# Kernel optimization log

Hardware: AMD Instinct MI355X
Metric: run time of the kernel (lower is better)

The kernel has to match this reference:

```python
import jax, jax.numpy as jnp
import numpy as np

N_NODES = 50000
N_EDGES = 800000
HEADS = 2
HID = 64
NEG_SLOPE = 0.2


def setup_inputs() -> dict:
    key = jax.random.key(0)
    ks = jax.random.split(key, 8)
    x = jax.random.normal(ks[0], (N_NODES, 128), dtype=jnp.float32)
    W_src = jax.random.normal(ks[1], (128, HEADS * HID), dtype=jnp.float32) * (1.0 / np.sqrt(128))
    W_dst = jax.random.normal(ks[2], (128, HEADS * HID), dtype=jnp.float32) * (1.0 / np.sqrt(128))
    att_src = jax.random.normal(ks[3], (HEADS, HID), dtype=jnp.float32) * 0.1
    att_dst = jax.random.normal(ks[4], (HEADS, HID), dtype=jnp.float32) * 0.1
    bias = jax.random.normal(ks[5], (HEADS * HID,), dtype=jnp.float32) * 0.01
    prelu_w = jnp.full((HEADS * HID,), 0.25, dtype=jnp.float32)
    edge_index = jax.random.randint(ks[6], (2, N_EDGES), 0, N_NODES, dtype=jnp.int64)
    return {"x": x, "W_src": W_src, "W_dst": W_dst, "att_src": att_src,
            "att_dst": att_dst, "bias": bias, "prelu_w": prelu_w,
            "edge_index": edge_index}


def gat_prelu(x, W_src, W_dst, att_src, att_dst, bias, prelu_w, edge_index):
    N = x.shape[0]
    src, dst = edge_index[0], edge_index[1]
    xs = (x @ W_src).reshape(N, HEADS, HID)   # [N,H,C]
    xd = (x @ W_dst).reshape(N, HEADS, HID)
    a_src = jnp.einsum('nhc,hc->nh', xs, att_src)  # [N,H]
    a_dst = jnp.einsum('nhc,hc->nh', xd, att_dst)
    e = jax.nn.leaky_relu(a_src[src] + a_dst[dst], NEG_SLOPE)  # [E,H]
    # segment softmax over incoming edges of each dst node
    m = jax.ops.segment_max(e, dst, num_segments=N)            # [N,H]
    ee = jnp.exp(e - m[dst])
    denom = jax.ops.segment_sum(ee, dst, num_segments=N)
    alpha = ee / (denom[dst] + 1e-16)                          # [E,H]
    msg = xs[src] * alpha[:, :, None]                          # [E,H,C]
    out = jax.ops.segment_sum(msg, dst, num_segments=N)        # [N,H,C]
    out = out.reshape(N, HEADS * HID) + bias
    return jnp.where(out >= 0, out, prelu_w * out)


def reference(x, W_src, W_dst, att_src, att_dst, bias, prelu_w, edge_index):
    return gat_prelu(x, W_src, W_dst, att_src, att_dst, bias, prelu_w, edge_index)
```

## Files before the change

kernel.cpp:

```cpp
#include <hip/hip_runtime.h>
#include <hip/hip_fp16.h>


#define N_NODES 50000
#define N_EDGES 800000
#define CAP     56
#define NB      49
#define CHUNK   2048
#define NBLK    391
#define CCAP    96

#define OFF_A      0
#define OFF_CNT    800000
#define OFF_XS     1000256
#define OFF_BKT    13800256
#define OFF_SWZ    36200256
#define DOUT_COARSE 0
#define DOUT_CELL   14714880

typedef _Float16 f16x8 __attribute__((ext_vector_type(8)));
typedef float    f32x4 __attribute__((ext_vector_type(4)));
typedef unsigned long long u64;

__global__ __launch_bounds__(256) void k0_prep(
    const float* __restrict__ Wsrc, const float* __restrict__ Wdst,
    const float* __restrict__ att_s, const float* __restrict__ att_d,
    __half* __restrict__ swz)
{
    __shared__ float vS[128 * 4];
    const int nt = blockIdx.x;
    const int t = threadIdx.x;
    if (nt == 8) {
        if (t < 128) {
            const float* wsp = Wsrc + t * 128;
            const float* wdp = Wdst + t * 128;
            float a0 = 0.f, a1 = 0.f, a2 = 0.f, a3 = 0.f;
#pragma unroll 8
            for (int c = 0; c < 64; ++c) {
                a0 += wsp[c]      * att_s[c];
                a1 += wsp[64 + c] * att_s[64 + c];
                a2 += wdp[c]      * att_d[c];
                a3 += wdp[64 + c] * att_d[64 + c];
            }
            *(float4*)(vS + t * 4) = make_float4(a0, a1, a2, a3);
        }
        __syncthreads();
    }
    const int kb = t >> 6, L = t & 63;
    const int col = L & 15;
    const int krow = kb * 32 + ((L >> 4) & 3) * 8;
    f16x8 v;
    if (nt < 8) {
#pragma unroll
        for (int j = 0; j < 8; ++j)
            v[j] = (_Float16)Wsrc[(size_t)(krow + j) * 128 + nt * 16 + col];
    } else {
#pragma unroll
        for (int j = 0; j < 8; ++j)
            v[j] = (col < 4) ? (_Float16)vS[(krow + j) * 4 + col] : (_Float16)0.f;
    }
    *(f16x8*)(swz + ((size_t)(kb * 9 + nt) * 64 + L) * 8) = v;
}

__global__ __launch_bounds__(256) void k1_gemm(
    const float* __restrict__ x, const __half* __restrict__ swz,
    __half* __restrict__ xs, float* __restrict__ a_all)
{
    const int t = threadIdx.x;
    const int w = t >> 6, L = t & 63;
    const int m = L & 15, q = L >> 4;
    const int n_a = blockIdx.x * 64 + w * 16 + m;
    const int rrow = (n_a < N_NODES) ? n_a : (N_NODES - 1);
    const float* xrow = x + (size_t)rrow * 128;

    f32x4 acc[9];
#pragma unroll
    for (int nt = 0; nt < 9; ++nt) acc[nt] = (f32x4){0.f, 0.f, 0.f, 0.f};

#pragma unroll
    for (int kb = 0; kb < 4; ++kb) {
        const int k0 = kb * 32 + q * 8;
        float4 xa = *(const float4*)(xrow + k0);
        float4 xb = *(const float4*)(xrow + k0 + 4);
        f16x8 a;
        a[0] = (_Float16)xa.x; a[1] = (_Float16)xa.y;
        a[2] = (_Float16)xa.z; a[3] = (_Float16)xa.w;
        a[4] = (_Float16)xb.x; a[5] = (_Float16)xb.y;
        a[6] = (_Float16)xb.z; a[7] = (_Float16)xb.w;
        const f16x8* bbase = (const f16x8*)swz + (size_t)(kb * 9) * 64 + L;
#pragma unroll
        for (int nt = 0; nt < 9; ++nt) {
            f16x8 b = bbase[(size_t)nt * 64];
            acc[nt] = __builtin_amdgcn_mfma_f32_16x16x32_f16(a, b, acc[nt], 0, 0, 0);
        }
    }

    const int rbase = blockIdx.x * 64 + w * 16 + q * 4;
#pragma unroll
    for (int nt = 0; nt < 8; ++nt) {
#pragma unroll
        for (int r = 0; r < 4; ++r) {
            int n = rbase + r;
            if (n < N_NODES)
                xs[(size_t)n * 128 + nt * 16 + m] = (__half)acc[nt][r];
        }
    }
    if (m < 4) {
#pragma unroll
        for (int r = 0; r < 4; ++r) {
            int n = rbase + r;
            if (n < N_NODES) a_all[(size_t)n * 4 + m] = acc[8][r];
        }
    }
}

__global__ __launch_bounds__(256) void kB_bin(
    const int* __restrict__ ei, const float* __restrict__ a_all,
    u64* __restrict__ coarse, int* __restrict__ cellcnt)
{
    __shared__ int lcnt[NB];
    const int t = threadIdx.x;
    if (t < NB) lcnt[t] = 0;
    __syncthreads();
    const int e0 = blockIdx.x * CHUNK;
#pragma unroll
    for (int u = 0; u < 8; ++u) {
        int e = e0 + u * 256 + t;
        if (e < N_EDGES) {
            int s = ei[e];
            int d = ei[N_EDGES + e];
            float2 as = *(const float2*)(a_all + (size_t)s * 4);
            float2 ad = *(const float2*)(a_all + (size_t)d * 4 + 2);
            float w0 = as.x + ad.x;
            float w1 = as.y + ad.y;
            w0 = (w0 >= 0.f) ? w0 : 0.2f * w0;
            w1 = (w1 >= 0.f) ? w1 : 0.2f * w1;
            __half2 hw = __floats2half2_rn(__expf(w0), __expf(w1));
            unsigned lo = (unsigned)s | ((unsigned)(d & 1023) << 16);
            u64 ent = (u64)lo | ((u64)*reinterpret_cast<unsigned*>(&hw) << 32);
            int b = d >> 10;
            int pos = atomicAdd(&lcnt[b], 1);
            if (pos < CCAP)
                coarse[((size_t)b * NBLK + blockIdx.x) * CCAP + pos] = ent;
        }
    }
    __syncthreads();
    if (t < NB) {
        int c = lcnt[t];
        cellcnt[t * NBLK + blockIdx.x] = (c < CCAP) ? c : CCAP;
    }
}

__global__ __launch_bounds__(1024) void kD_fine(
    const u64* __restrict__ coarse, const int* __restrict__ cellcnt,
    int* __restrict__ cnt, int2* __restrict__ bkt)
{
    __shared__ int cur[1024];
    __shared__ int ccnt[NBLK];
    const int b = blockIdx.x, t = threadIdx.x;
    cur[t] = 0;
    if (t < NBLK) ccnt[t] = cellcnt[b * NBLK + t];
    __syncthreads();
    const u64* src = coarse + (size_t)b * NBLK * CCAP;
    for (int g = t; g < NBLK * CCAP; g += 1024) {
        int c = g / CCAP, s = g - c * CCAP;
        if (s < ccnt[c]) {
            u64 ent = src[g];
            unsigned lo = (unsigned)ent;
            int drel = (lo >> 16) & 1023;
            int pos = atomicAdd(&cur[drel], 1);
            if (pos < CAP) {
                int d = (b << 10) + drel;
                bkt[(size_t)d * CAP + pos] =
                    make_int2((int)(lo & 0xFFFF), (int)(unsigned)(ent >> 32));
            }
        }
    }
    __syncthreads();
    {
        int d = (b << 10) + t;
        if (d < N_NODES) cnt[d] = cur[t];
    }
}

template<bool GUARD>
__device__ __forceinline__ void step8(const int2* __restrict__ row, int k, int m,
                                      int sh, int j, const __half* __restrict__ xs,
                                      float& ax, float& ay, float& sw)
{
    int4 p0 = *(const int4*)(row + k);
    int4 p1 = *(const int4*)(row + k + 2);
    int4 p2 = *(const int4*)(row + k + 4);
    int4 p3 = *(const int4*)(row + k + 6);
    int s0 = p0.x, s1 = p0.z, s2 = p1.x, s3 = p1.z;
    int s4 = p2.x, s5 = p2.z, s6 = p3.x, s7 = p3.z;
    unsigned w0 = (unsigned)p0.y, w1 = (unsigned)p0.w;
    unsigned w2 = (unsigned)p1.y, w3 = (unsigned)p1.w;
    unsigned w4 = (unsigned)p2.y, w5 = (unsigned)p2.w;
    unsigned w6 = (unsigned)p3.y, w7 = (unsigned)p3.w;
    if (GUARD) {
        if (k + 0 >= m) { s0 = 0; w0 = 0; }
        if (k + 1 >= m) { s1 = 0; w1 = 0; }
        if (k + 2 >= m) { s2 = 0; w2 = 0; }
        if (k + 3 >= m) { s3 = 0; w3 = 0; }
        if (k + 4 >= m) { s4 = 0; w4 = 0; }
        if (k + 5 >= m) { s5 = 0; w5 = 0; }
        if (k + 6 >= m) { s6 = 0; w6 = 0; }
        if (k + 7 >= m) { s7 = 0; w7 = 0; }
    }
    __half2 h0 = *(const __half2*)(xs + (size_t)s0 * 128 + j);
    __half2 h1 = *(const __half2*)(xs + (size_t)s1 * 128 + j);
    __half2 h2 = *(const __half2*)(xs + (size_t)s2 * 128 + j);
    __half2 h3 = *(const __half2*)(xs + (size_t)s3 * 128 + j);
    __half2 h4 = *(const __half2*)(xs + (size_t)s4 * 128 + j);
    __half2 h5 = *(const __half2*)(xs + (size_t)s5 * 128 + j);
    __half2 h6 = *(const __half2*)(xs + (size_t)s6 * 128 + j);
    __half2 h7 = *(const __half2*)(xs + (size_t)s7 * 128 + j);
    float a0 = __half2float(__ushort_as_half((unsigned short)(w0 >> sh)));
    float a1 = __half2float(__ushort_as_half((unsigned short)(w1 >> sh)));
    float a2 = __half2float(__ushort_as_half((unsigned short)(w2 >> sh)));
    float a3 = __half2float(__ushort_as_half((unsigned short)(w3 >> sh)));
    float a4 = __half2float(__ushort_as_half((unsigned short)(w4 >> sh)));
    float a5 = __half2float(__ushort_as_half((unsigned short)(w5 >> sh)));
    float a6 = __half2float(__ushort_as_half((unsigned short)(w6 >> sh)));
    float a7 = __half2float(__ushort_as_half((unsigned short)(w7 >> sh)));
    ax += __half2float(h0.x) * a0; ay += __half2float(h0.y) * a0;
    ax += __half2float(h1.x) * a1; ay += __half2float(h1.y) * a1;
    ax += __half2float(h2.x) * a2; ay += __half2float(h2.y) * a2;
    ax += __half2float(h3.x) * a3; ay += __half2float(h3.y) * a3;
    ax += __half2float(h4.x) * a4; ay += __half2float(h4.y) * a4;
    ax += __half2float(h5.x) * a5; ay += __half2float(h5.y) * a5;
    ax += __half2float(h6.x) * a6; ay += __half2float(h6.y) * a6;
    ax += __half2float(h7.x) * a7; ay += __half2float(h7.y) * a7;
    sw += ((a0 + a1) + (a2 + a3)) + ((a4 + a5) + (a6 + a7));
}

__global__ __launch_bounds__(256) void k6_agg(
    const int2* __restrict__ bkt, const int* __restrict__ cnt,
    const __half* __restrict__ xs, const float* __restrict__ bias,
    const float* __restrict__ prelu_w, float* __restrict__ out)
{
    const int n = blockIdx.x * 4 + (threadIdx.x >> 6);
    const int lane = threadIdx.x & 63;
    const int j = lane * 2;
    const int sh = (lane >> 5) * 16;
    int m = cnt[n]; if (m > CAP) m = CAP;
    const int2* row = bkt + (size_t)n * CAP;
    float ax = 0.f, ay = 0.f, sw = 0.f;
    int k = 0;
    for (; k + 8 <= m; k += 8)
        step8<false>(row, k, m, sh, j, xs, ax, ay, sw);
    if (k < m)
        step8<true>(row, k, m, sh, j, xs, ax, ay, sw);

    float inv = 1.f / (sw + 1e-16f);
    float o0 = ax * inv + bias[j];
    float o1 = ay * inv + bias[j + 1];
    float2 r;
    r.x = (o0 >= 0.f) ? o0 : prelu_w[j] * o0;
    r.y = (o1 >= 0.f) ? o1 : prelu_w[j + 1] * o1;
    *(float2*)(out + (size_t)n * 128 + j) = r;
}

extern "C" void kernel_launch(void* const* d_in, const int* in_sizes, int n_in,
                              void* d_out, int out_size, void* d_ws, size_t ws_size,
                              hipStream_t stream) {
    const float* x      = (const float*)d_in[0];
    const float* Wsrc   = (const float*)d_in[1];
    const float* Wdst   = (const float*)d_in[2];
    const float* att_s  = (const float*)d_in[3];
    const float* att_d  = (const float*)d_in[4];
    const float* bias   = (const float*)d_in[5];
    const float* prelu  = (const float*)d_in[6];
    const int*   ei     = (const int*)d_in[7];
    float* out = (float*)d_out;

    char* ws = (char*)d_ws;
    float*  a_all  = (float*)(ws + OFF_A);
    int*    cnt    = (int*)(ws + OFF_CNT);
    __half* xs     = (__half*)(ws + OFF_XS);
    int2*   bkt    = (int2*)(ws + OFF_BKT);
    __half* swz    = (__half*)(ws + OFF_SWZ);

    char* outb = (char*)d_out;
    u64* coarse  = (u64*)(outb + DOUT_COARSE);
    int* cellcnt = (int*)(outb + DOUT_CELL);

    k0_prep<<<9, 256, 0, stream>>>(Wsrc, Wdst, att_s, att_d, swz);
    k1_gemm<<<(N_NODES + 63) / 64, 256, 0, stream>>>(x, swz, xs, a_all);
    kB_bin<<<NBLK, 256, 0, stream>>>(ei, a_all, coarse, cellcnt);
    kD_fine<<<NB, 1024, 0, stream>>>(coarse, cellcnt, cnt, bkt);
    k6_agg<<<N_NODES / 4, 256, 0, stream>>>(bkt, cnt, xs, bias, prelu, out);
}
```

Measured before the change: 185.8 us.

## Stage GEMM output through LDS, vectorize binning loads, double chunk size

The GEMM epilogue now writes the fp16 projection into a shared-memory tile and then stores full 16-byte rows to global memory, replacing scattered 2-byte stores. The binning kernel handles two edges per thread with int2 index loads, and the chunk size is doubled with larger per-cell capacity, which halves the number of blocks and cells. The fine-bucketing kernel reads coarse entries in pairs with 16-byte loads. The aim is fewer, wider memory transactions. The cost is extra LDS use and a sync in the GEMM, plus fewer binning blocks, which lowers parallelism and may overflow the per-cell capacity.

Measured after the change: 179.2 us. 1.04x faster.

```diff
diff --git a/kernel.cpp b/kernel.cpp
--- a/kernel.cpp
+++ b/kernel.cpp
@@ -6,9 +6,9 @@
 #define N_EDGES 800000
 #define CAP     56
 #define NB      49
-#define CHUNK   2048
-#define NBLK    391
-#define CCAP    96
+#define CHUNK   4096
+#define NBLK    196
+#define CCAP    160
 
 #define OFF_A      0
 #define OFF_CNT    800000
@@ -16,7 +16,7 @@
 #define OFF_BKT    13800256
 #define OFF_SWZ    36200256
 #define DOUT_COARSE 0
-#define DOUT_CELL   14714880
+#define DOUT_CELL   12293120
 
 typedef _Float16 f16x8 __attribute__((ext_vector_type(8)));
 typedef float    f32x4 __attribute__((ext_vector_type(4)));
@@ -66,6 +66,7 @@
     const float* __restrict__ x, const __half* __restrict__ swz,
     __half* __restrict__ xs, float* __restrict__ a_all)
 {
+    __shared__ __half tile[64 * 136];
     const int t = threadIdx.x;
     const int w = t >> 6, L = t & 63;
     const int m = L & 15, q = L >> 4;
@@ -95,20 +96,30 @@
         }
     }
 
-    const int rbase = blockIdx.x * 64 + w * 16 + q * 4;
+    const int rloc = w * 16 + q * 4;
 #pragma unroll
     for (int nt = 0; nt < 8; ++nt) {
 #pragma unroll
+        for (int r = 0; r < 4; ++r)
+            tile[(rloc + r) * 136 + nt * 16 + m] = (__half)acc[nt][r];
+    }
+    __syncthreads();
+    const int n0 = blockIdx.x * 64;
+#pragma unroll
+    for (int cc = 0; cc < 4; ++cc) {
+        int task = cc * 256 + t;
+        int row = task >> 4, ch = (task & 15) * 8;
+        int n = n0 + row;
+        if (n < N_NODES) {
+            ulonglong2 v = *(const ulonglong2*)(tile + row * 136 + ch);
+            *(ulonglong2*)(xs + (size_t)n * 128 + ch) = v;
+        }
+    }
+
+    if (m < 4) {
+#pragma unroll
         for (int r = 0; r < 4; ++r) {
-            int n = rbase + r;
-            if (n < N_NODES)
-                xs[(size_t)n * 128 + nt * 16 + m] = (__half)acc[nt][r];
-        }
-    }
-    if (m < 4) {
-#pragma unroll
-        for (int r = 0; r < 4; ++r) {
-            int n = rbase + r;
+            int n = n0 + rloc + r;
             if (n < N_NODES) a_all[(size_t)n * 4 + m] = acc[8][r];
         }
     }
@@ -125,23 +136,33 @@
     const int e0 = blockIdx.x * CHUNK;
 #pragma unroll
     for (int u = 0; u < 8; ++u) {
-        int e = e0 + u * 256 + t;
+        int e = e0 + u * 512 + t * 2;
         if (e < N_EDGES) {
-            int s = ei[e];
-            int d = ei[N_EDGES + e];
-            float2 as = *(const float2*)(a_all + (size_t)s * 4);
-            float2 ad = *(const float2*)(a_all + (size_t)d * 4 + 2);
-            float w0 = as.x + ad.x;
-            float w1 = as.y + ad.y;
-            w0 = (w0 >= 0.f) ? w0 : 0.2f * w0;
-            w1 = (w1 >= 0.f) ? w1 : 0.2f * w1;
-            __half2 hw = __floats2half2_rn(__expf(w0), __expf(w1));
-            unsigned lo = (unsigned)s | ((unsigned)(d & 1023) << 16);
-            u64 ent = (u64)lo | ((u64)*reinterpret_cast<unsigned*>(&hw) << 32);
-            int b = d >> 10;
-            int pos = atomicAdd(&lcnt[b], 1);
-            if (pos < CCAP)
-                coarse[((size_t)b * NBLK + blockIdx.x) * CCAP + pos] = ent;
+            int2 ss = *(const int2*)(ei + e);
+            int2 dd = *(const int2*)(ei + N_EDGES + e);
+            float2 as0 = *(const float2*)(a_all + (size_t)ss.x * 4);
+            float2 ad0 = *(const float2*)(a_all + (size_t)dd.x * 4 + 2);
+            float2 as1 = *(const float2*)(a_all + (size_t)ss.y * 4);
+            float2 ad1 = *(const float2*)(a_all + (size_t)dd.y * 4 + 2);
+            float e00 = as0.x + ad0.x, e01 = as0.y + ad0.y;
+            float e10 = as1.x + ad1.x, e11 = as1.y + ad1.y;
+            e00 = (e00 >= 0.f) ? e00 : 0.2f * e00;
+            e01 = (e01 >= 0.f) ? e01 : 0.2f * e01;
+            e10 = (e10 >= 0.f) ? e10 : 0.2f * e10;
+            e11 = (e11 >= 0.f) ? e11 : 0.2f * e11;
+            __half2 hw0 = __floats2half2_rn(__expf(e00), __expf(e01));
+            __half2 hw1 = __floats2half2_rn(__expf(e10), __expf(e11));
+            unsigned lo0 = (unsigned)ss.x | ((unsigned)(dd.x & 1023) << 16);
+            unsigned lo1 = (unsigned)ss.y | ((unsigned)(dd.y & 1023) << 16);
+            u64 ent0 = (u64)lo0 | ((u64)*reinterpret_cast<unsigned*>(&hw0) << 32);
+            u64 ent1 = (u64)lo1 | ((u64)*reinterpret_cast<unsigned*>(&hw1) << 32);
+            int b0 = dd.x >> 10, b1 = dd.y >> 10;
+            int p0 = atomicAdd(&lcnt[b0], 1);
+            int p1 = atomicAdd(&lcnt[b1], 1);
+            if (p0 < CCAP)
+                coarse[((size_t)b0 * NBLK + blockIdx.x) * CCAP + p0] = ent0;
+            if (p1 < CCAP)
+                coarse[((size_t)b1 * NBLK + blockIdx.x) * CCAP + p1] = ent1;
         }
     }
     __syncthreads();
@@ -162,17 +183,31 @@
     if (t < NBLK) ccnt[t] = cellcnt[b * NBLK + t];
     __syncthreads();
     const u64* src = coarse + (size_t)b * NBLK * CCAP;
-    for (int g = t; g < NBLK * CCAP; g += 1024) {
-        int c = g / CCAP, s = g - c * CCAP;
-        if (s < ccnt[c]) {
-            u64 ent = src[g];
-            unsigned lo = (unsigned)ent;
-            int drel = (lo >> 16) & 1023;
-            int pos = atomicAdd(&cur[drel], 1);
-            if (pos < CAP) {
-                int d = (b << 10) + drel;
-                bkt[(size_t)d * CAP + pos] =
-                    make_int2((int)(lo & 0xFFFF), (int)(unsigned)(ent >> 32));
+    const int HALF = CCAP / 2;
+    for (int g2 = t; g2 < NBLK * HALF; g2 += 1024) {
+        int c = g2 / HALF, sp = (g2 - c * HALF) * 2;
+        int cc = ccnt[c];
+        if (sp < cc) {
+            ulonglong2 pr = *(const ulonglong2*)(src + (size_t)c * CCAP + sp);
+            {
+                unsigned lo = (unsigned)pr.x;
+                int drel = (lo >> 16) & 1023;
+                int pos = atomicAdd(&cur[drel], 1);
+                if (pos < CAP) {
+                    int d = (b << 10) + drel;
+                    bkt[(size_t)d * CAP + pos] =
+                        make_int2((int)(lo & 0xFFFF), (int)(unsigned)(pr.x >> 32));
+                }
+            }
+            if (sp + 1 < cc) {
+                unsigned lo = (unsigned)pr.y;
+                int drel = (lo >> 16) & 1023;
+                int pos = atomicAdd(&cur[drel], 1);
+                if (pos < CAP) {
+                    int d = (b << 10) + drel;
+                    bkt[(size_t)d * CAP + pos] =
+                        make_int2((int)(lo & 0xFFFF), (int)(unsigned)(pr.y >> 32));
+                }
             }
         }
     }
```
